# Performance work log

Measured on AMD Instinct MI355X. Metric: run time of the kernel, lower is better.

## Reference

```python
import jax, jax.numpy as jnp
import numpy as np

N = 50000   # nodes per node type
D = 128     # in/out channels
E = 500000  # edges per edge type


def setup_inputs() -> dict:
    key = jax.random.key(0)
    ks = jax.random.split(key, 24)
    s = 1.0 / np.sqrt(D)
    def w(k, shape):
        return jax.random.normal(k, shape, jnp.float32) * s
    inp = {
        "x_a": jax.random.normal(ks[0], (N, D), jnp.float32),
        "x_b": jax.random.normal(ks[1], (N, D), jnp.float32),
        "edge_e1": jax.random.randint(ks[2], (2, E), 0, N),  # a -> b
        "edge_e2": jax.random.randint(ks[3], (2, E), 0, N),  # b -> a
        "edge_e3": jax.random.randint(ks[4], (2, E), 0, N),  # b -> a
    }
    i = 5
    for e in ("e1", "e2", "e3"):
        inp[f"Ws_{e}"] = w(ks[i], (D, D)); i += 1
        inp[f"Wt_{e}"] = w(ks[i], (D, D)); i += 1
        inp[f"wih_{e}"] = w(ks[i], (3 * D, D)); i += 1
        inp[f"whh_{e}"] = w(ks[i], (3 * D, D)); i += 1
        inp[f"bih_{e}"] = jnp.zeros((3 * D,), jnp.float32)
        inp[f"bhh_{e}"] = jnp.zeros((3 * D,), jnp.float32)
    return inp


def _gru_cell(x, h, wih, whh, bih, bhh):
    # PyTorch nn.GRUCell semantics: x = input, h = hidden
    gi = x @ wih.T + bih
    gh = h @ whh.T + bhh
    ir, iz, inn = jnp.split(gi, 3, axis=1)
    hr, hz, hn = jnp.split(gh, 3, axis=1)
    r = jax.nn.sigmoid(ir + hr)
    z = jax.nn.sigmoid(iz + hz)
    n = jnp.tanh(inn + r * hn)
    return (1.0 - z) * n + z * h


def _edge_type(x_src, x_tgt, edge, Ws, Wt, wih, whh, bih, bhh):
    sx = x_src @ Ws.T                       # [Ns, D] per-edge-type source linear (no bias)
    tx = x_tgt @ Wt.T                       # [Nt, D] per-edge-type target linear
    msg = sx[edge[0]]                       # [E, D]  gather by source index
    agg = jax.ops.segment_sum(msg, edge[1], num_segments=x_tgt.shape[0])  # scatter-sum
    return _gru_cell(tx, agg, wih, whh, bih, bhh)


def reference(x_a, x_b, edge_e1, edge_e2, edge_e3,
              Ws_e1, Wt_e1, wih_e1, whh_e1, bih_e1, bhh_e1,
              Ws_e2, Wt_e2, wih_e2, whh_e2, bih_e2, bhh_e2,
              Ws_e3, Wt_e3, wih_e3, whh_e3, bih_e3, bhh_e3):
    # edge type e1: a -> b  (div['b'] = 1)
    out_b = _edge_type(x_a, x_b, edge_e1, Ws_e1, Wt_e1, wih_e1, whh_e1, bih_e1, bhh_e1)
    # edge types e2, e3: b -> a  (div['a'] = 2)
    out_a = _edge_type(x_b, x_a, edge_e2, Ws_e2, Wt_e2, wih_e2, whh_e2, bih_e2, bhh_e2)
    out_a = out_a + _edge_type(x_b, x_a, edge_e3, Ws_e3, Wt_e3, wih_e3, whh_e3, bih_e3, bhh_e3)
    out_a = out_a / 2.0
    out_a = jax.nn.relu(out_a)
    out_b = jax.nn.relu(out_b)
    return jnp.stack([out_a, out_b])  # [2, N, D]
```

## Files before the change

kernel.cpp:

```cpp
#include <hip/hip_runtime.h>
#include <hip/hip_bf16.h>
#include <stdint.h>
#include <math.h>

#define NN 50000
#define DD 128
#define EE 500000
#define ROWT 1563
#define NBIN 98
#define CHB 245

typedef __attribute__((ext_vector_type(8))) short bfx8;
typedef __attribute__((ext_vector_type(4))) short bfx4;
typedef __attribute__((ext_vector_type(4))) float f32x4;
typedef __attribute__((ext_vector_type(4))) int i32x4;
typedef unsigned short u16;

static __device__ __forceinline__ short f2bf(float f) {
  union { float f; uint32_t u; } v; v.f = f;
  uint32_t r = (v.u + 0x7fffu + ((v.u >> 16) & 1u)) >> 16;
  return (short)r;
}
static __device__ __forceinline__ float bf2f(short b) {
  union { uint32_t u; float f; } v; v.u = ((uint32_t)(uint16_t)b) << 16;
  return v.f;
}

static __device__ __forceinline__ void gl_lds16(const short* g, short* l) {
  __builtin_amdgcn_global_load_lds(
      (const __attribute__((address_space(1))) unsigned int*)g,
      (__attribute__((address_space(3))) unsigned int*)l, 16, 0, 0);
}

static __device__ __forceinline__ bfx8 load_pk(const short* p, int ct, int ks, int lane) {
  return *reinterpret_cast<const bfx8*>(p + ((((size_t)ct * 4 + ks) * 64 + lane) << 3));
}

struct PrepArgs {
  const float* csrc[2]; short* cdst[2];
  const float* A[6]; const float* B[6]; short* pout[6];
  const float* psrc[3]; short* pdst[3];
  const int* edge[3]; int* ccnt;
};

__global__ __launch_bounds__(256) void k_prep(PrepArgs p) {
  const int y = blockIdx.y;
  if (y < 2) {
    int i = (blockIdx.x * 256 + threadIdx.x) * 4;
    if (i >= NN * DD) return;
    f32x4 v = *reinterpret_cast<const f32x4*>(p.csrc[y] + i);
    bfx4 o;
    o[0]=f2bf(v[0]); o[1]=f2bf(v[1]); o[2]=f2bf(v[2]); o[3]=f2bf(v[3]);
    *reinterpret_cast<bfx4*>(p.cdst[y] + i) = o;
  } else if (y < 8) {
    if (blockIdx.x >= 192) return;
    const int e = y - 2;
    const float* A = p.A[e];
    const float* B = p.B[e];
    int tid = blockIdx.x * 256 + threadIdx.x;
    int i = tid >> 7, j = tid & 127;
    float acc = 0.f;
    #pragma unroll 4
    for (int k = 0; k < 128; ++k) acc += A[i * 128 + k] * B[k * 128 + j];
    int ct = i >> 4;
    int lane = (i & 15) | ((((j & 31) >> 3)) << 4);
    int ks = j >> 5;
    int elem = j & 7;
    p.pout[e][(((size_t)(ct * 4 + ks) * 64 + lane) << 3) + elem] = f2bf(acc);
  } else if (y < 11) {
    if (blockIdx.x >= 8) return;
    const int jb = y - 8;
    int tid = blockIdx.x * 256 + threadIdx.x;
    int lane = tid & 63, ks = (tid >> 6) & 3, ct = tid >> 8;
    const float* s = p.psrc[jb] + (size_t)(ct * 16 + (lane & 15)) * 128 + ks * 32 + ((lane >> 4) << 3);
    bfx8 o;
    #pragma unroll
    for (int i = 0; i < 8; ++i) o[i] = f2bf(s[i]);
    *reinterpret_cast<bfx8*>(p.pdst[jb] + ((size_t)tid << 3)) = o;
  } else {
    if (blockIdx.x >= CHB) return;
    const int t = y - 11, tid = threadIdx.x;
    __shared__ int cnt[NBIN];
    for (int b = tid; b < NBIN; b += 256) cnt[b] = 0;
    __syncthreads();
    const int* ed = p.edge[t];
    int base = blockIdx.x * 2048;
    #pragma unroll
    for (int m = 0; m < 8; ++m) {
      int i = base + m * 256 + tid;
      if (i < EE) atomicAdd(&cnt[ed[EE + i] >> 9], 1);
    }
    __syncthreads();
    for (int b = tid; b < NBIN; b += 256)
      if (cnt[b]) atomicAdd(&p.ccnt[t * NBIN + b], cnt[b]);
  }
}

struct CsrArgs {
  const int* edge[3];
  int* ccnt;
  int* cstart;
  int* ccur;
  uint32_t* cbkt[3];
  int* offs[3];
  u16* bucket[3];
};

__global__ __launch_bounds__(384) void k_cscan(CsrArgs a) {
  __shared__ int buf[3][128];
  int ty = threadIdx.x >> 7;
  int i = threadIdx.x & 127;
  int v = (i < NBIN) ? a.ccnt[ty * NBIN + i] : 0;
  buf[ty][i] = v;
  __syncthreads();
  for (int off = 1; off < 128; off <<= 1) {
    int tv = (i >= off) ? buf[ty][i - off] : 0;
    __syncthreads();
    buf[ty][i] += tv;
    __syncthreads();
  }
  if (i < NBIN) {
    int excl = buf[ty][i] - v;
    a.cstart[ty * NBIN + i] = excl;
    a.ccur[ty * NBIN + i] = excl;
  }
}

__global__ __launch_bounds__(256) void k_cbin(CsrArgs a) {
  const int t = blockIdx.y, tid = threadIdx.x;
  __shared__ int cnt[NBIN], cur[NBIN];
  for (int b = tid; b < NBIN; b += 256) cnt[b] = 0;
  __syncthreads();
  const int* ed = a.edge[t];
  int base = blockIdx.x * 4096;
  #pragma unroll
  for (int m = 0; m < 16; ++m) {
    int i = base + m * 256 + tid;
    if (i < EE) atomicAdd(&cnt[ed[EE + i] >> 9], 1);
  }
  __syncthreads();
  for (int b = tid; b < NBIN; b += 256)
    cur[b] = cnt[b] ? atomicAdd(&a.ccur[t * NBIN + b], cnt[b]) : 0;
  __syncthreads();
  uint32_t* cb = a.cbkt[t];
  #pragma unroll
  for (int m = 0; m < 16; ++m) {
    int i = base + m * 256 + tid;
    if (i < EE) {
      int tg = ed[EE + i];
      int b = tg >> 9;
      int pos = atomicAdd(&cur[b], 1);
      cb[pos] = (uint32_t)ed[i] | ((uint32_t)(tg & 511) << 20);
    }
  }
}

__global__ __launch_bounds__(256) void k_fsort(CsrArgs a) {
  const int t = blockIdx.y, bin = blockIdx.x, tid = threadIdx.x;
  __shared__ int rc[512], rcur[512], sb[256];
  int s0 = a.cstart[t * NBIN + bin];
  int cntb = a.ccnt[t * NBIN + bin];
  rc[tid] = 0; rc[tid + 256] = 0;
  __syncthreads();
  const uint32_t* cb = a.cbkt[t];
  for (int i = tid; i < cntb; i += 256) atomicAdd(&rc[cb[s0 + i] >> 20], 1);
  __syncthreads();
  int A = rc[2 * tid], B = rc[2 * tid + 1], s = A + B;
  sb[tid] = s;
  __syncthreads();
  for (int off = 1; off < 256; off <<= 1) {
    int v = (tid >= off) ? sb[tid - off] : 0;
    __syncthreads();
    sb[tid] += v;
    __syncthreads();
  }
  int excl = sb[tid] - s;
  rcur[2 * tid] = s0 + excl;
  rcur[2 * tid + 1] = s0 + excl + A;
  int rows0 = bin << 9;
  int nr = NN - rows0; if (nr > 512) nr = 512;
  if (2 * tid < nr)     a.offs[t][rows0 + 2 * tid]     = s0 + excl + A;
  if (2 * tid + 1 < nr) a.offs[t][rows0 + 2 * tid + 1] = s0 + excl + A + B;
  __syncthreads();
  u16* fb = a.bucket[t];
  for (int i = tid; i < cntb; i += 256) {
    uint32_t e = cb[s0 + i];
    int pos = atomicAdd(&rcur[e >> 20], 1);
    fb[pos] = (u16)e;
  }
}

struct GArgs {
  const int* offs[3]; const u16* bkt[3];
  const short* xsrc[3]; short* agg[3];
};

__global__ __launch_bounds__(256) void k_gather(GArgs a) {
  const int ty = blockIdx.y;
  const int* __restrict__ offs = a.offs[ty];
  const u16* __restrict__ bucket = a.bkt[ty];
  const short* __restrict__ xsrc = a.xsrc[ty];
  short* __restrict__ agg = a.agg[ty];
  int tid = threadIdx.x;
  int row = blockIdx.x * 32 + (tid >> 3);
  if (row >= NN) return;
  int c0 = (tid & 7) * 16;
  int start = row ? offs[row - 1] : 0;
  int end = offs[row];
  f32x4 s0 = (f32x4)(0.f), s1 = (f32x4)(0.f), s2 = (f32x4)(0.f), s3 = (f32x4)(0.f);
  int i = start;
  for (; i + 8 <= end; i += 8) {
    const short* pp[8];
    #pragma unroll
    for (int m = 0; m < 8; ++m) pp[m] = xsrc + (size_t)bucket[i + m] * DD + c0;
    #pragma unroll
    for (int m = 0; m < 8; ++m) {
      bfx8 u = *reinterpret_cast<const bfx8*>(pp[m]);
      bfx8 v = *reinterpret_cast<const bfx8*>(pp[m] + 8);
      #pragma unroll
      for (int j = 0; j < 4; ++j) {
        s0[j] += bf2f(u[j]); s1[j] += bf2f(u[4+j]);
        s2[j] += bf2f(v[j]); s3[j] += bf2f(v[4+j]);
      }
    }
  }
  for (; i + 4 <= end; i += 4) {
    const short* pp[4];
    #pragma unroll
    for (int m = 0; m < 4; ++m) pp[m] = xsrc + (size_t)bucket[i + m] * DD + c0;
    #pragma unroll
    for (int m = 0; m < 4; ++m) {
      bfx8 u = *reinterpret_cast<const bfx8*>(pp[m]);
      bfx8 v = *reinterpret_cast<const bfx8*>(pp[m] + 8);
      #pragma unroll
      for (int j = 0; j < 4; ++j) {
        s0[j] += bf2f(u[j]); s1[j] += bf2f(u[4+j]);
        s2[j] += bf2f(v[j]); s3[j] += bf2f(v[4+j]);
      }
    }
  }
  for (; i < end; ++i) {
    const short* p = xsrc + (size_t)bucket[i] * DD + c0;
    bfx8 u = *reinterpret_cast<const bfx8*>(p), v = *reinterpret_cast<const bfx8*>(p + 8);
    #pragma unroll
    for (int j = 0; j < 4; ++j) {
      s0[j] += bf2f(u[j]); s1[j] += bf2f(u[4+j]);
      s2[j] += bf2f(v[j]); s3[j] += bf2f(v[4+j]);
    }
  }
  short* d = agg + (size_t)row * DD + c0;
  bfx8 o0, o1;
  #pragma unroll
  for (int j = 0; j < 4; ++j) {
    o0[j] = f2bf(s0[j]); o0[4+j] = f2bf(s1[j]);
    o1[j] = f2bf(s2[j]); o1[4+j] = f2bf(s3[j]);
  }
  *reinterpret_cast<bfx8*>(d) = o0;
  *reinterpret_cast<bfx8*>(d + 8) = o1;
}

static __device__ __forceinline__ void gru8(const f32x4 h[2], const f32x4 ai[2][3],
                                            const f32x4 ah[2][3],
                                            float bir, float biz, float bin,
                                            float bhr, float bhz, float bhn,
                                            f32x4 res[2]) {
  #pragma unroll
  for (int rf = 0; rf < 2; ++rf)
    #pragma unroll
    for (int q = 0; q < 4; ++q) {
      float ir = ai[rf][0][q] + bir, iz = ai[rf][1][q] + biz, in = ai[rf][2][q] + bin;
      float hr = ah[rf][0][q] + bhr, hz = ah[rf][1][q] + bhz, hn = ah[rf][2][q] + bhn;
      float rr = __builtin_amdgcn_rcpf(1.f + __expf(-(ir + hr)));
      float zz = __builtin_amdgcn_rcpf(1.f + __expf(-(iz + hz)));
      float t2 = in + rr * hn;
      float nn = 1.f - 2.f * __builtin_amdgcn_rcpf(__expf(2.f * t2) + 1.f);
      res[rf][q] = (1.f - zz) * nn + zz * h[rf][q];
    }
}

static __device__ __forceinline__ void gru_unit(
    const short* lds, int gbase, int ctw, int lane,
    const short* wsp, const short* combp, const short* whhsp,
    f32x4 (&h)[2], f32x4 (&ai)[2][3], f32x4 (&ah)[2][3]) {
  #pragma unroll
  for (int rf = 0; rf < 2; ++rf) {
    h[rf] = (f32x4)(0.f);
    #pragma unroll
    for (int g = 0; g < 3; ++g) { ai[rf][g] = (f32x4)(0.f); ah[rf][g] = (f32x4)(0.f); }
  }
  #pragma unroll
  for (int ks = 0; ks < 4; ++ks) {
    bfx8 x0 = *reinterpret_cast<const bfx8*>(lds + (0 + ks) * 512 + lane * 8);
    bfx8 x1 = *reinterpret_cast<const bfx8*>(lds + (4 + ks) * 512 + lane * 8);
    bfx8 g0 = *reinterpret_cast<const bfx8*>(lds + (gbase + ks) * 512 + lane * 8);
    bfx8 g1 = *reinterpret_cast<const bfx8*>(lds + (gbase + 4 + ks) * 512 + lane * 8);
    bfx8 bws = load_pk(wsp, ctw, ks, lane);
    h[0] = __builtin_amdgcn_mfma_f32_16x16x32_bf16(g0, bws, h[0], 0, 0, 0);
    h[1] = __builtin_amdgcn_mfma_f32_16x16x32_bf16(g1, bws, h[1], 0, 0, 0);
    #pragma unroll
    for (int g = 0; g < 3; ++g) {
      int ct = g * 8 + ctw;
      bfx8 bi = load_pk(combp, ct, ks, lane);
      bfx8 bh = load_pk(whhsp, ct, ks, lane);
      ai[0][g] = __builtin_amdgcn_mfma_f32_16x16x32_bf16(x0, bi, ai[0][g], 0, 0, 0);
      ai[1][g] = __builtin_amdgcn_mfma_f32_16x16x32_bf16(x1, bi, ai[1][g], 0, 0, 0);
      ah[0][g] = __builtin_amdgcn_mfma_f32_16x16x32_bf16(g0, bh, ah[0][g], 0, 0, 0);
      ah[1][g] = __builtin_amdgcn_mfma_f32_16x16x32_bf16(g1, bh, ah[1][g], 0, 0, 0);
    }
  }
}

struct GGArgs {
  const short* agg1; const short* agg2; const short* agg3;
  const short* xa; const short* xb;
  const short* wsp1; const short* combp1; const short* whhsp1;
  const short* wsp2; const short* combp2; const short* whhsp2;
  const short* wsp3; const short* combp3; const short* whhsp3;
  const float* bih1; const float* bhh1;
  const float* bih2; const float* bhh2;
  const float* bih3; const float* bhh3;
  float* out_a; float* out_b;
};

__global__ __launch_bounds__(512) void k_ggru(GGArgs a) {
  __shared__ short lds[24 * 512];
  __shared__ float r3buf[32 * 68];
  const int wave = threadIdx.x >> 6, lane = threadIdx.x & 63;
  const int bx = blockIdx.x;

  if (bx < 2 * ROWT) {
    const int rbase = (bx >> 1) * 32;
    const int colblk = bx & 1;
    const int unit = wave >> 2;
    const int ctw = colblk * 4 + (wave & 3);

    #pragma unroll
    for (int i = 0; i < 3; ++i) {
      int f = wave * 3 + i;
      const short* src = (f < 8) ? a.xa : ((f < 16) ? a.agg2 : a.agg3);
      int r = rbase + ((f >> 2) & 1) * 16 + (lane & 15);
      if (r >= NN) r = NN - 1;
      gl_lds16(src + (size_t)r * DD + (f & 3) * 32 + ((lane >> 4) << 3), lds + f * 512);
    }
    __syncthreads();

    const short* wspU   = unit ? a.wsp3   : a.wsp2;
    const short* combpU = unit ? a.combp3 : a.combp2;
    const short* whhspU = unit ? a.whhsp3 : a.whhsp2;
    const float* bihU   = unit ? a.bih3   : a.bih2;
    const float* bhhU   = unit ? a.bhh3   : a.bhh2;
    const int gbase = unit ? 16 : 8;

    f32x4 h[2], ai[2][3], ah[2][3];
    gru_unit(lds, gbase, ctw, lane, wspU, combpU, whhspU, h, ai, ah);

    const int col = ctw * 16 + (lane & 15);
    const int cl = (wave & 3) * 16 + (lane & 15);
    const int lq = (lane >> 4) << 2;
    f32x4 res[2];
    gru8(h, ai, ah, bihU[col], bihU[128 + col], bihU[256 + col],
         bhhU[col], bhhU[128 + col], bhhU[256 + col], res);

    if (unit == 1) {
      #pragma unroll
      for (int rf = 0; rf < 2; ++rf)
        #pragma unroll
        for (int q = 0; q < 4; ++q)
          r3buf[(rf * 16 + lq + q) * 68 + cl] = res[rf][q];
    }
    __syncthreads();
    if (unit == 0) {
      #pragma unroll
      for (int rf = 0; rf < 2; ++rf)
        #pragma unroll
        for (int q = 0; q < 4; ++q) {
          int r = rbase + rf * 16 + lq + q;
          if (r < NN) {
            float r3 = r3buf[(rf * 16 + lq + q) * 68 + cl];
            a.out_a[(size_t)r * DD + col] = fmaxf((res[rf][q] + r3) * 0.5f, 0.f);
          }
        }
    }
  } else {
    const int rbase = (bx - 2 * ROWT) * 32;
    const int ctw = wave;

    #pragma unroll
    for (int i = 0; i < 2; ++i) {
      int f = wave * 2 + i;
      const short* src = (f & 8) ? a.agg1 : a.xb;
      int r = rbase + ((f >> 2) & 1) * 16 + (lane & 15);
      if (r >= NN) r = NN - 1;
      gl_lds16(src + (size_t)r * DD + (f & 3) * 32 + ((lane >> 4) << 3), lds + f * 512);
    }
    __syncthreads();

    f32x4 h[2], ai[2][3], ah[2][3];
    gru_unit(lds, 8, ctw, lane, a.wsp1, a.combp1, a.whhsp1, h, ai, ah);

    const int col = ctw * 16 + (lane & 15);
    f32x4 res[2];
    gru8(h, ai, ah, a.bih1[col], a.bih1[128 + col], a.bih1[256 + col],
         a.bhh1[col], a.bhh1[128 + col], a.bhh1[256 + col], res);
    const int lq = (lane >> 4) << 2;
    #pragma unroll
    for (int rf = 0; rf < 2; ++rf)
      #pragma unroll
      for (int q = 0; q < 4; ++q) {
        int r = rbase + rf * 16 + lq + q;
        if (r < NN) a.out_b[(size_t)r * DD + col] = fmaxf(res[rf][q], 0.f);
      }
  }
}

extern "C" void kernel_launch(void* const* d_in, const int* in_sizes, int n_in,
                              void* d_out, int out_size, void* d_ws, size_t ws_size,
                              hipStream_t stream) {
  const float* x_a = (const float*)d_in[0];
  const float* x_b = (const float*)d_in[1];
  const int* edges[3] = {(const int*)d_in[2], (const int*)d_in[3], (const int*)d_in[4]};
  const float *Ws[3], *Wt[3], *wih[3], *whh[3], *bih[3], *bhh[3];
  for (int e = 0; e < 3; ++e) {
    int b = 5 + e * 6;
    Ws[e]  = (const float*)d_in[b + 0];
    Wt[e]  = (const float*)d_in[b + 1];
    wih[e] = (const float*)d_in[b + 2];
    whh[e] = (const float*)d_in[b + 3];
    bih[e] = (const float*)d_in[b + 4];
    bhh[e] = (const float*)d_in[b + 5];
  }

  char* ws = (char*)d_ws;
  short* xa_bf  = (short*)ws;
  short* xb_bf  = (short*)(ws + 12800000);
  short* aggX   = (short*)(ws + 25600000);
  int*   offs   = (int*)(ws + 64000000);
  u16*   bucket = (u16*)(ws + 64600000);
  uint32_t* cbkt= (uint32_t*)(ws + 67600000);
  short* pk     = (short*)(ws + 73600000);
  int*   ccnt   = (int*)(ws + 74300000);
  int*   cstart = (int*)(ws + 74310000);
  int*   ccur   = (int*)(ws + 74320000);
  short *wsp[3], *combp[3], *whhsp[3];
  short* aggp[3];
  int* offsp[3]; u16* bktp[3]; uint32_t* cbktp[3];
  for (int e = 0; e < 3; ++e) {
    short* base = pk + (size_t)e * 114688;
    wsp[e] = base; combp[e] = base + 16384; whhsp[e] = base + 65536;
    aggp[e]  = aggX + (size_t)e * NN * DD;
    offsp[e] = offs + (size_t)e * 50000;
    bktp[e]  = bucket + (size_t)e * 500000;
    cbktp[e] = cbkt + (size_t)e * 500000;
  }

  (void)hipMemsetAsync(ccnt, 0, 3 * NBIN * sizeof(int), stream);

  PrepArgs pa;
  pa.csrc[0] = x_a; pa.cdst[0] = xa_bf;
  pa.csrc[1] = x_b; pa.cdst[1] = xb_bf;
  for (int e = 0; e < 3; ++e) {
    pa.A[e] = wih[e];     pa.B[e] = Wt[e]; pa.pout[e] = combp[e];
    pa.A[3 + e] = whh[e]; pa.B[3 + e] = Ws[e]; pa.pout[3 + e] = whhsp[e];
    pa.psrc[e] = Ws[e];   pa.pdst[e] = wsp[e];
    pa.edge[e] = edges[e];
  }
  pa.ccnt = ccnt;
  hipLaunchKernelGGL(k_prep, dim3(6250, 14), dim3(256), 0, stream, pa);

  CsrArgs ca;
  for (int e = 0; e < 3; ++e) {
    ca.edge[e] = edges[e];
    ca.cbkt[e] = cbktp[e];
    ca.offs[e] = offsp[e];
    ca.bucket[e] = bktp[e];
  }
  ca.ccnt = ccnt; ca.cstart = cstart; ca.ccur = ccur;
  hipLaunchKernelGGL(k_cscan, dim3(1), dim3(384), 0, stream, ca);
  hipLaunchKernelGGL(k_cbin, dim3((EE + 4095) / 4096, 3), dim3(256), 0, stream, ca);
  hipLaunchKernelGGL(k_fsort, dim3(NBIN, 3), dim3(256), 0, stream, ca);

  GArgs ga;
  const short* srcb[3] = {xa_bf, xb_bf, xb_bf};
  for (int e = 0; e < 3; ++e) {
    ga.offs[e] = offsp[e]; ga.bkt[e] = bktp[e];
    ga.xsrc[e] = srcb[e];  ga.agg[e] = aggp[e];
  }
  hipLaunchKernelGGL(k_gather, dim3(ROWT, 3), dim3(256), 0, stream, ga);

  float* out_a = (float*)d_out;
  float* out_b = (float*)d_out + (size_t)NN * DD;

  GGArgs gg;
  gg.agg1 = aggp[0]; gg.agg2 = aggp[1]; gg.agg3 = aggp[2];
  gg.xa = xa_bf; gg.xb = xb_bf;
  gg.wsp1 = wsp[0]; gg.combp1 = combp[0]; gg.whhsp1 = whhsp[0];
  gg.wsp2 = wsp[1]; gg.combp2 = combp[1]; gg.whhsp2 = whhsp[1];
  gg.wsp3 = wsp[2]; gg.combp3 = combp[2]; gg.whhsp3 = whhsp[2];
  gg.bih1 = bih[0]; gg.bhh1 = bhh[0];
  gg.bih2 = bih[1]; gg.bhh2 = bhh[1];
  gg.bih3 = bih[2]; gg.bhh3 = bhh[2];
  gg.out_a = out_a; gg.out_b = out_b;
  hipLaunchKernelGGL(k_ggru, dim3(ROWT * 3), dim3(512), 0, stream, gg);
}
```

Measured before the change: 207.8 us.

## Compute both a-side GRU units per wave instead of splitting across waves

Changes the a-side GRU blocks so that each of the 8 waves covers all 128 columns' worth of column tiles and computes both the e2 and e3 GRU units sequentially in registers. Previously, half the waves did e2 and half e3 and combined them through an LDS buffer and a barrier. This removes the r3buf LDS exchange, the extra __syncthreads and one third of the blocks (grid drops from 3*ROWT to 2*ROWT), and each 32-row tile is now loaded once. In exchange, each a-side block does twice the work with fewer blocks, and register pressure may rise from holding both results.

```diff
diff --git a/kernel.cpp b/kernel.cpp
--- a/kernel.cpp
+++ b/kernel.cpp
@@ -324,15 +324,14 @@
 
 __global__ __launch_bounds__(512) void k_ggru(GGArgs a) {
   __shared__ short lds[24 * 512];
-  __shared__ float r3buf[32 * 68];
   const int wave = threadIdx.x >> 6, lane = threadIdx.x & 63;
   const int bx = blockIdx.x;
-
-  if (bx < 2 * ROWT) {
-    const int rbase = (bx >> 1) * 32;
-    const int colblk = bx & 1;
-    const int unit = wave >> 2;
-    const int ctw = colblk * 4 + (wave & 3);
+  const int ctw = wave;
+  const int col = ctw * 16 + (lane & 15);
+  const int lq = (lane >> 4) << 2;
+
+  if (bx < ROWT) {
+    const int rbase = bx * 32;
 
     #pragma unroll
     for (int i = 0; i < 3; ++i) {
@@ -344,46 +343,30 @@
     }
     __syncthreads();
 
-    const short* wspU   = unit ? a.wsp3   : a.wsp2;
-    const short* combpU = unit ? a.combp3 : a.combp2;
-    const short* whhspU = unit ? a.whhsp3 : a.whhsp2;
-    const float* bihU   = unit ? a.bih3   : a.bih2;
-    const float* bhhU   = unit ? a.bhh3   : a.bhh2;
-    const int gbase = unit ? 16 : 8;
-
-    f32x4 h[2], ai[2][3], ah[2][3];
-    gru_unit(lds, gbase, ctw, lane, wspU, combpU, whhspU, h, ai, ah);
-
-    const int col = ctw * 16 + (lane & 15);
-    const int cl = (wave & 3) * 16 + (lane & 15);
-    const int lq = (lane >> 4) << 2;
-    f32x4 res[2];
-    gru8(h, ai, ah, bihU[col], bihU[128 + col], bihU[256 + col],
-         bhhU[col], bhhU[128 + col], bhhU[256 + col], res);
-
-    if (unit == 1) {
+    f32x4 res2[2];
+    {
+      f32x4 h[2], ai[2][3], ah[2][3];
+      gru_unit(lds, 8, ctw, lane, a.wsp2, a.combp2, a.whhsp2, h, ai, ah);
+      gru8(h, ai, ah, a.bih2[col], a.bih2[128 + col], a.bih2[256 + col],
+           a.bhh2[col], a.bhh2[128 + col], a.bhh2[256 + col], res2);
+    }
+    f32x4 res3[2];
+    {
+      f32x4 h[2], ai[2][3], ah[2][3];
+      gru_unit(lds, 16, ctw, lane, a.wsp3, a.combp3, a.whhsp3, h, ai, ah);
+      gru8(h, ai, ah, a.bih3[col], a.bih3[128 + col], a.bih3[256 + col],
+           a.bhh3[col], a.bhh3[128 + col], a.bhh3[256 + col], res3);
+    }
+    #pragma unroll
+    for (int rf = 0; rf < 2; ++rf)
       #pragma unroll
-      for (int rf = 0; rf < 2; ++rf)
-        #pragma unroll
-        for (int q = 0; q < 4; ++q)
-          r3buf[(rf * 16 + lq + q) * 68 + cl] = res[rf][q];
-    }
-    __syncthreads();
-    if (unit == 0) {
-      #pragma unroll
-      for (int rf = 0; rf < 2; ++rf)
-        #pragma unroll
-        for (int q = 0; q < 4; ++q) {
-          int r = rbase + rf * 16 + lq + q;
-          if (r < NN) {
-            float r3 = r3buf[(rf * 16 + lq + q) * 68 + cl];
-            a.out_a[(size_t)r * DD + col] = fmaxf((res[rf][q] + r3) * 0.5f, 0.f);
-          }
-        }
-    }
+      for (int q = 0; q < 4; ++q) {
+        int r = rbase + rf * 16 + lq + q;
+        if (r < NN)
+          a.out_a[(size_t)r * DD + col] = fmaxf((res2[rf][q] + res3[rf][q]) * 0.5f, 0.f);
+      }
   } else {
-    const int rbase = (bx - 2 * ROWT) * 32;
-    const int ctw = wave;
+    const int rbase = (bx - ROWT) * 32;
 
     #pragma unroll
     for (int i = 0; i < 2; ++i) {
@@ -398,11 +381,9 @@
     f32x4 h[2], ai[2][3], ah[2][3];
     gru_unit(lds, 8, ctw, lane, a.wsp1, a.combp1, a.whhsp1, h, ai, ah);
 
-    const int col = ctw * 16 + (lane & 15);
     f32x4 res[2];
     gru8(h, ai, ah, a.bih1[col], a.bih1[128 + col], a.bih1[256 + col],
          a.bhh1[col], a.bhh1[128 + col], a.bhh1[256 + col], res);
-    const int lq = (lane >> 4) << 2;
     #pragma unroll
     for (int rf = 0; rf < 2; ++rf)
       #pragma unroll
@@ -500,5 +481,5 @@
   gg.bih2 = bih[1]; gg.bhh2 = bhh[1];
   gg.bih3 = bih[2]; gg.bhh3 = bhh[2];
   gg.out_a = out_a; gg.out_b = out_b;
-  hipLaunchKernelGGL(k_ggru, dim3(ROWT * 3), dim3(512), 0, stream, gg);
-}
+  hipLaunchKernelGGL(k_ggru, dim3(ROWT * 2), dim3(512), 0, stream, gg);
+}
```

Measured after the change: 225.6 us. 8.6% more time.
